# Kernel optimization log

Hardware: AMD Instinct MI355X
Metric: run time of the kernel (lower is better)

The kernel has to match this reference:

```python
import jax, jax.numpy as jnp
import numpy as np

D_MODEL = 1024
NUM_EXPERTS = 8
TOP_K = 2


def setup_inputs() -> dict:
    key = jax.random.key(0)
    k_x, k_g, k_w1, k_w2 = jax.random.split(key, 4)
    B, S, D, E = 4, 2048, D_MODEL, NUM_EXPERTS
    s_in = 1.0 / np.sqrt(D)
    s_hid = 1.0 / np.sqrt(4 * D)
    return {
        "x": jax.random.normal(k_x, (B, S, D), dtype=jnp.float32),
        "gate_w": jax.random.uniform(k_g, (E, D), jnp.float32, -s_in, s_in),
        "w1": jax.random.uniform(k_w1, (E, 4 * D, D), jnp.float32, -s_in, s_in),
        "w2": jax.random.uniform(k_w2, (E, D, 4 * D), jnp.float32, -s_hid, s_hid),
    }


def reference(x, gate_w, w1, w2):
    # x: [B,S,D]; gate_w: [E,D]; w1: [E,4D,D]; w2: [E,D,4D]
    gate_logits = jnp.einsum("bsd,ed->bse", x, gate_w)  # [B,S,E]
    top_v, top_i = jax.lax.top_k(gate_logits, TOP_K)     # [B,S,K]
    gates = jax.nn.softmax(top_v, axis=-1)               # [B,S,K]
    # combine weights per expert: [B,S,E]
    combine = jnp.sum(
        jax.nn.one_hot(top_i, NUM_EXPERTS, dtype=x.dtype) * gates[..., None],
        axis=-2,
    )
    out = jnp.zeros_like(x)
    for e in range(NUM_EXPERTS):
        h = jax.nn.relu(jnp.einsum("bsd,fd->bsf", x, w1[e]))   # [B,S,4D]
        y = jnp.einsum("bsf,df->bsd", h, w2[e])                # [B,S,D]
        out = out + combine[..., e, None] * y
    return out
```

## Files before the change

kernel.cpp:

```cpp
#include <hip/hip_runtime.h>
#include <hip/hip_bf16.h>
#include <stdint.h>

#define D_MODEL 1024
#define HDIM    4096
#define NE      8
#define MAXTILES 136

typedef __attribute__((ext_vector_type(8))) short short8;
typedef __attribute__((ext_vector_type(4))) float f32x4;
typedef __attribute__((ext_vector_type(2))) __bf16 bf16x2;
typedef __attribute__((ext_vector_type(4))) unsigned int uint4v;
typedef __attribute__((ext_vector_type(2))) unsigned int uint2v;

__device__ inline unsigned pk2(float a, float b) {
  bf16x2 v; v[0] = (__bf16)a; v[1] = (__bf16)b;
  return __builtin_bit_cast(unsigned, v);
}
__device__ inline unsigned short f2bf(float a) {
  __bf16 v = (__bf16)a;
  return __builtin_bit_cast(unsigned short, v);
}
__device__ inline void async16(const void* g, void* l) {
  __builtin_amdgcn_global_load_lds(
      (const __attribute__((address_space(1))) unsigned int*)g,
      (__attribute__((address_space(3))) unsigned int*)l, 16, 0, 0);
}

__global__ __launch_bounds__(256) void gate_kernel(
    const float* __restrict__ x, const float* __restrict__ gw,
    int* __restrict__ counts, int* __restrict__ tk_e, float* __restrict__ tk_g,
    unsigned short* __restrict__ xbf)
{
  const int t = blockIdx.x;
  const int tid = threadIdx.x;
  const float4 xv = ((const float4*)(x + (size_t)t * D_MODEL))[tid];
  if (xbf) {
    uint2v p; p[0] = pk2(xv.x, xv.y); p[1] = pk2(xv.z, xv.w);
    ((uint2v*)(xbf + (size_t)t * D_MODEL))[tid] = p;
  }
  float part[NE];
#pragma unroll
  for (int e = 0; e < NE; ++e) {
    const float4 gv = ((const float4*)(gw + e * D_MODEL))[tid];
    part[e] = xv.x * gv.x + xv.y * gv.y + xv.z * gv.z + xv.w * gv.w;
  }
#pragma unroll
  for (int off = 32; off > 0; off >>= 1)
#pragma unroll
    for (int e = 0; e < NE; ++e) part[e] += __shfl_down(part[e], off, 64);
  __shared__ float red[4][NE];
  const int wid = tid >> 6, lane = tid & 63;
  if (lane == 0)
    for (int e = 0; e < NE; ++e) red[wid][e] = part[e];
  __syncthreads();
  if (tid == 0) {
    float lg[NE];
    for (int e = 0; e < NE; ++e) lg[e] = red[0][e] + red[1][e] + red[2][e] + red[3][e];
    int e0 = 0;
    for (int e = 1; e < NE; ++e) if (lg[e] > lg[e0]) e0 = e;
    int e1 = (e0 == 0) ? 1 : 0;
    for (int e = 0; e < NE; ++e) { if (e == e0) continue; if (lg[e] > lg[e1]) e1 = e; }
    const float g0 = 1.0f / (1.0f + expf(lg[e1] - lg[e0]));
    tk_e[2*t] = e0; tk_e[2*t+1] = e1;
    tk_g[2*t] = g0; tk_g[2*t+1] = 1.0f - g0;
    atomicAdd(&counts[e0], 1);
    atomicAdd(&counts[e1], 1);
  }
}

__global__ void prefix_kernel(const int* __restrict__ counts,
                              int* __restrict__ cursor, int* __restrict__ offsets,
                              int* __restrict__ tiles, int* __restrict__ n_tiles) {
  if (threadIdx.x == 0) {
    int s = 0, n = 0;
    for (int e = 0; e < NE; ++e) {
      offsets[e] = s;
      const int nt = (counts[e] + 127) >> 7;
      for (int z = 0; z < nt; ++z) tiles[n++] = (e << 16) | z;
      s += counts[e];
      cursor[e] = 0;
    }
    *n_tiles = n;
  }
}

__global__ __launch_bounds__(256) void place_kernel(
    const int* __restrict__ tk_e, const float* __restrict__ tk_g,
    const int* __restrict__ offsets, int* __restrict__ cursor,
    int* __restrict__ token_of, float* __restrict__ gate_of, int T)
{
  const int t = blockIdx.x * 256 + threadIdx.x;
  if (t >= T) return;
  for (int k = 0; k < 2; ++k) {
    const int e = tk_e[2*t + k];
    const int pos = offsets[e] + atomicAdd(&cursor[e], 1);
    token_of[pos] = t;
    gate_of[pos] = tk_g[2*t + k];
  }
}

__global__ __launch_bounds__(256) void convert_kernel(
    const float* __restrict__ src, unsigned short* __restrict__ dst, long n4)
{
  long i = (long)blockIdx.x * 256 + threadIdx.x;
  const long stride = (long)gridDim.x * 256;
  for (; i < n4; i += stride) {
    const float4 v = ((const float4*)src)[i];
    uint2v p; p[0] = pk2(v.x, v.y); p[1] = pk2(v.z, v.w);
    ((uint2v*)dst)[i] = p;
  }
}

template<bool ABF, bool BBF>
__global__ __launch_bounds__(256) void gemm1_t(
    const float* __restrict__ xf, const unsigned short* __restrict__ xb,
    const float* __restrict__ w1f, const unsigned short* __restrict__ w1b,
    const int* __restrict__ counts, const int* __restrict__ offsets,
    const int* __restrict__ tiles, const int* __restrict__ n_tiles,
    const int* __restrict__ token_of, unsigned short* __restrict__ h)
{
  if ((int)blockIdx.x >= *n_tiles) return;
  const int desc = tiles[blockIdx.x];
  const int e = desc >> 16, zt = desc & 0xffff;
  const int ne = counts[e];
  const int off = offsets[e];
  const int p0 = off + zt * 128, pend = off + ne;
  const int f0 = blockIdx.y * 128;

  __shared__ __align__(16) short As[128 * 32];
  __shared__ __align__(16) short Bs[128 * 32];

  const int tid = threadIdx.x, lane = tid & 63, wid = tid >> 6;
  const int wm = (wid & 1) * 64, wn = (wid >> 1) * 64;
  const int lr = lane & 15, lq = lane >> 4;

  const unsigned short* aSrc0 = nullptr; const unsigned short* aSrc1 = nullptr;
  short* aDst0 = nullptr; short* aDst1 = nullptr;
  const float* aptrF = nullptr;
  if (ABF) {
    const int r0 = wid * 32 + (lane >> 2), r1 = r0 + 16;
    int i0 = p0 + r0; if (i0 >= pend) i0 = pend - 1;
    int i1 = p0 + r1; if (i1 >= pend) i1 = pend - 1;
    aSrc0 = xb + (size_t)token_of[i0] * D_MODEL + (lane & 3) * 8;
    aSrc1 = xb + (size_t)token_of[i1] * D_MODEL + (lane & 3) * 8;
    aDst0 = As + (wid * 2 + 0) * 512;
    aDst1 = As + (wid * 2 + 1) * 512;
  } else {
    const int r = tid >> 1, ch = tid & 1;
    int ip = p0 + r; if (ip >= pend) ip = pend - 1;
    aptrF = xf + (size_t)token_of[ip] * D_MODEL + ch * 16;
  }
  const unsigned short* bSrc0 = nullptr; const unsigned short* bSrc1 = nullptr;
  short* bDst0 = nullptr; short* bDst1 = nullptr;
  const float* bptrF = nullptr;
  if (BBF) {
    const unsigned short* w1be = w1b + (size_t)e * ((size_t)HDIM * D_MODEL);
    const int r0 = wid * 32 + (lane >> 2), r1 = r0 + 16;
    bSrc0 = w1be + (size_t)(f0 + r0) * D_MODEL + (lane & 3) * 8;
    bSrc1 = w1be + (size_t)(f0 + r1) * D_MODEL + (lane & 3) * 8;
    bDst0 = Bs + (wid * 2 + 0) * 512;
    bDst1 = Bs + (wid * 2 + 1) * 512;
  } else {
    const float* w1fe = w1f + (size_t)e * ((size_t)HDIM * D_MODEL);
    const int r = tid >> 1, ch = tid & 1;
    bptrF = w1fe + (size_t)(f0 + r) * D_MODEL + ch * 16;
  }
  const int rM = tid >> 1, chM = tid & 1;

  f32x4 acc[4][4];
#pragma unroll
  for (int i = 0; i < 4; ++i)
#pragma unroll
    for (int j = 0; j < 4; ++j) acc[i][j] = (f32x4){0.f, 0.f, 0.f, 0.f};

  for (int kk = 0; kk < D_MODEL; kk += 32) {
    float4 a0, a1, a2, a3, b0, b1, b2, b3;
    if (!ABF) {
      a0 = *(const float4*)(aptrF + kk);     a1 = *(const float4*)(aptrF + kk + 4);
      a2 = *(const float4*)(aptrF + kk + 8); a3 = *(const float4*)(aptrF + kk + 12);
    }
    if (!BBF) {
      b0 = *(const float4*)(bptrF + kk);     b1 = *(const float4*)(bptrF + kk + 4);
      b2 = *(const float4*)(bptrF + kk + 8); b3 = *(const float4*)(bptrF + kk + 12);
    }
    __syncthreads();
    if (ABF) {
      async16(aSrc0 + kk, aDst0);
      async16(aSrc1 + kk, aDst1);
    } else {
      uint4v wa0 = {pk2(a0.x,a0.y), pk2(a0.z,a0.w), pk2(a1.x,a1.y), pk2(a1.z,a1.w)};
      uint4v wa1 = {pk2(a2.x,a2.y), pk2(a2.z,a2.w), pk2(a3.x,a3.y), pk2(a3.z,a3.w)};
      *(uint4v*)&As[rM * 32 + chM * 16]     = wa0;
      *(uint4v*)&As[rM * 32 + chM * 16 + 8] = wa1;
    }
    if (BBF) {
      async16(bSrc0 + kk, bDst0);
      async16(bSrc1 + kk, bDst1);
    } else {
      uint4v wb0 = {pk2(b0.x,b0.y), pk2(b0.z,b0.w), pk2(b1.x,b1.y), pk2(b1.z,b1.w)};
      uint4v wb1 = {pk2(b2.x,b2.y), pk2(b2.z,b2.w), pk2(b3.x,b3.y), pk2(b3.z,b3.w)};
      *(uint4v*)&Bs[rM * 32 + chM * 16]     = wb0;
      *(uint4v*)&Bs[rM * 32 + chM * 16 + 8] = wb1;
    }
    __syncthreads();
    short8 af[4], bfr[4];
#pragma unroll
    for (int i = 0; i < 4; ++i) af[i]  = *(const short8*)&As[(wm + i*16 + lr) * 32 + lq * 8];
#pragma unroll
    for (int j = 0; j < 4; ++j) bfr[j] = *(const short8*)&Bs[(wn + j*16 + lr) * 32 + lq * 8];
#pragma unroll
    for (int i = 0; i < 4; ++i)
#pragma unroll
      for (int j = 0; j < 4; ++j)
        acc[i][j] = __builtin_amdgcn_mfma_f32_16x16x32_bf16(af[i], bfr[j], acc[i][j], 0, 0, 0);
  }

#pragma unroll
  for (int i = 0; i < 4; ++i) {
#pragma unroll
    for (int g = 0; g < 4; ++g) {
      const int m = wm + i*16 + lq*4 + g;
      const int pp = p0 + m;
      if (pp < pend) {
        unsigned short* hrow = h + (size_t)pp * HDIM + f0 + wn + lr;
#pragma unroll
        for (int j = 0; j < 4; ++j) {
          float v = acc[i][j][g];
          v = v > 0.f ? v : 0.f;
          hrow[j*16] = f2bf(v);
        }
      }
    }
  }
}

template<bool BBF>
__global__ __launch_bounds__(256) void gemm2_t(
    const unsigned short* __restrict__ h, const float* __restrict__ w2f,
    const unsigned short* __restrict__ w2b,
    const int* __restrict__ counts, const int* __restrict__ offsets,
    const int* __restrict__ tiles, const int* __restrict__ n_tiles,
    const int* __restrict__ token_of, const float* __restrict__ gate_of,
    float* __restrict__ out)
{
  if ((int)blockIdx.x >= *n_tiles) return;
  const int desc = tiles[blockIdx.x];
  const int e = desc >> 16, zt = desc & 0xffff;
  const int ne = counts[e];
  const int off = offsets[e];
  const int p0 = off + zt * 128, pend = off + ne;
  const int d0 = blockIdx.y * 128;

  __shared__ __align__(16) short As[128 * 32];
  __shared__ __align__(16) short Bs[128 * 32];

  const int tid = threadIdx.x, lane = tid & 63, wid = tid >> 6;
  const int wm = (wid & 1) * 64, wn = (wid >> 1) * 64;
  const int lr = lane & 15, lq = lane >> 4;

  const int rA0 = wid * 32 + (lane >> 2), rA1 = rA0 + 16;
  int iA0 = p0 + rA0; if (iA0 >= pend) iA0 = pend - 1;
  int iA1 = p0 + rA1; if (iA1 >= pend) iA1 = pend - 1;
  const unsigned short* aSrc0 = h + (size_t)iA0 * HDIM + (lane & 3) * 8;
  const unsigned short* aSrc1 = h + (size_t)iA1 * HDIM + (lane & 3) * 8;
  short* aDst0 = As + (wid * 2 + 0) * 512;
  short* aDst1 = As + (wid * 2 + 1) * 512;

  const unsigned short* bSrc0 = nullptr; const unsigned short* bSrc1 = nullptr;
  short* bDst0 = nullptr; short* bDst1 = nullptr;
  const float* bptrF = nullptr;
  if (BBF) {
    const unsigned short* w2be = w2b + (size_t)e * ((size_t)D_MODEL * HDIM);
    bSrc0 = w2be + (size_t)(d0 + rA0) * HDIM + (lane & 3) * 8;
    bSrc1 = w2be + (size_t)(d0 + rA1) * HDIM + (lane & 3) * 8;
    bDst0 = Bs + (wid * 2 + 0) * 512;
    bDst1 = Bs + (wid * 2 + 1) * 512;
  } else {
    const float* w2fe = w2f + (size_t)e * ((size_t)D_MODEL * HDIM);
    bptrF = w2fe + (size_t)(d0 + (tid >> 1)) * HDIM + (tid & 1) * 16;
  }
  const int rM = tid >> 1, chM = tid & 1;

  f32x4 acc[4][4];
#pragma unroll
  for (int i = 0; i < 4; ++i)
#pragma unroll
    for (int j = 0; j < 4; ++j) acc[i][j] = (f32x4){0.f, 0.f, 0.f, 0.f};

  for (int kk = 0; kk < HDIM; kk += 32) {
    float4 b0, b1, b2, b3;
    if (!BBF) {
      b0 = *(const float4*)(bptrF + kk);     b1 = *(const float4*)(bptrF + kk + 4);
      b2 = *(const float4*)(bptrF + kk + 8); b3 = *(const float4*)(bptrF + kk + 12);
    }
    __syncthreads();
    async16(aSrc0 + kk, aDst0);
    async16(aSrc1 + kk, aDst1);
    if (BBF) {
      async16(bSrc0 + kk, bDst0);
      async16(bSrc1 + kk, bDst1);
    } else {
      uint4v wb0 = {pk2(b0.x,b0.y), pk2(b0.z,b0.w), pk2(b1.x,b1.y), pk2(b1.z,b1.w)};
      uint4v wb1 = {pk2(b2.x,b2.y), pk2(b2.z,b2.w), pk2(b3.x,b3.y), pk2(b3.z,b3.w)};
      *(uint4v*)&Bs[rM * 32 + chM * 16]     = wb0;
      *(uint4v*)&Bs[rM * 32 + chM * 16 + 8] = wb1;
    }
    __syncthreads();
    short8 af[4], bfr[4];
#pragma unroll
    for (int i = 0; i < 4; ++i) af[i]  = *(const short8*)&As[(wm + i*16 + lr) * 32 + lq * 8];
#pragma unroll
    for (int j = 0; j < 4; ++j) bfr[j] = *(const short8*)&Bs[(wn + j*16 + lr) * 32 + lq * 8];
#pragma unroll
    for (int i = 0; i < 4; ++i)
#pragma unroll
      for (int j = 0; j < 4; ++j)
        acc[i][j] = __builtin_amdgcn_mfma_f32_16x16x32_bf16(af[i], bfr[j], acc[i][j], 0, 0, 0);
  }

#pragma unroll
  for (int i = 0; i < 4; ++i) {
#pragma unroll
    for (int g = 0; g < 4; ++g) {
      const int m = wm + i*16 + lq*4 + g;
      const int pp = p0 + m;
      if (pp < pend) {
        const int tok = token_of[pp];
        const float gv = gate_of[pp];
        float* orow = out + (size_t)tok * D_MODEL + d0 + wn + lr;
#pragma unroll
        for (int j = 0; j < 4; ++j)
          atomicAdd(&orow[j*16], gv * acc[i][j][g]);
      }
    }
  }
}

extern "C" void kernel_launch(void* const* d_in, const int* in_sizes, int n_in,
                              void* d_out, int out_size, void* d_ws, size_t ws_size,
                              hipStream_t stream)
{
  const float* x  = (const float*)d_in[0];
  const float* gw = (const float*)d_in[1];
  const float* w1 = (const float*)d_in[2];
  const float* w2 = (const float*)d_in[3];
  float* out = (float*)d_out;
  const int T = in_sizes[0] / D_MODEL;

  char* wsb = (char*)d_ws;
  int*   counts   = (int*)wsb;
  int*   cursor   = counts + 8;
  int*   offsets  = cursor + 8;
  int*   n_tiles  = offsets + 8;
  int*   tiles    = n_tiles + 1;
  int*   tk_e     = tiles + MAXTILES;
  float* tk_g     = (float*)(tk_e + 2*T);
  int*   token_of = (int*)(tk_g + 2*T);
  float* gate_of  = (float*)(token_of + 2*T);

  const size_t MB = 1u << 20;
  const size_t xbf_sz = (size_t)T * D_MODEL * 2;
  const size_t wbf_sz = (size_t)NE * HDIM * D_MODEL * 2;
  const size_t h_sz   = (size_t)(2*T) * HDIM * 2;

  const bool tierB = ws_size >= MB + xbf_sz + h_sz;
  const bool tierA = ws_size >= MB + xbf_sz + 2*wbf_sz + h_sz;

  unsigned short* xbf = tierB ? (unsigned short*)(wsb + MB) : nullptr;
  unsigned short* w1b = tierA ? (unsigned short*)(wsb + MB + xbf_sz) : nullptr;
  unsigned short* w2b = tierA ? (unsigned short*)(wsb + MB + xbf_sz + wbf_sz) : nullptr;
  unsigned short* h;
  if (tierA)      h = (unsigned short*)(wsb + MB + xbf_sz + 2*wbf_sz);
  else if (tierB) h = (unsigned short*)(wsb + MB + xbf_sz);
  else            h = (unsigned short*)(wsb + MB);

  hipMemsetAsync(d_ws, 0, 128, stream);
  hipMemsetAsync(d_out, 0, (size_t)out_size * sizeof(float), stream);

  gate_kernel<<<T, 256, 0, stream>>>(x, gw, counts, tk_e, tk_g, xbf);
  prefix_kernel<<<1, 64, 0, stream>>>(counts, cursor, offsets, tiles, n_tiles);
  place_kernel<<<(T + 255) / 256, 256, 0, stream>>>(tk_e, tk_g, offsets, cursor,
                                                    token_of, gate_of, T);
  if (tierA) {
    const long n4 = (long)NE * HDIM * D_MODEL / 4;
    convert_kernel<<<4096, 256, 0, stream>>>(w1, w1b, n4);
    convert_kernel<<<4096, 256, 0, stream>>>(w2, w2b, n4);
  }

  dim3 g1(MAXTILES, HDIM / 128, 1);
  dim3 g2(MAXTILES, D_MODEL / 128, 1);
  if (tierA) {
    gemm1_t<true, true><<<g1, 256, 0, stream>>>(x, xbf, w1, w1b, counts, offsets,
                                                tiles, n_tiles, token_of, h);
    gemm2_t<true><<<g2, 256, 0, stream>>>(h, w2, w2b, counts, offsets,
                                          tiles, n_tiles, token_of, gate_of, out);
  } else if (tierB) {
    gemm1_t<true, false><<<g1, 256, 0, stream>>>(x, xbf, w1, w1b, counts, offsets,
                                                 tiles, n_tiles, token_of, h);
    gemm2_t<false><<<g2, 256, 0, stream>>>(h, w2, w2b, counts, offsets,
                                           tiles, n_tiles, token_of, gate_of, out);
  } else {
    gemm1_t<false, false><<<g1, 256, 0, stream>>>(x, xbf, w1, w1b, counts, offsets,
                                                  tiles, n_tiles, token_of, h);
    gemm2_t<false><<<g2, 256, 0, stream>>>(h, w2, w2b, counts, offsets,
                                           tiles, n_tiles, token_of, gate_of, out);
  }
}
```

Baseline: 1.058 ms.

## Replace atomic scatter in expert GEMM2 with per-slot stores plus gather reduce

In the bf16-weights path, the second expert GEMM no longer atomically adds gated results into the output. It writes raw per-slot rows into a workspace buffer instead, and a new reduce kernel gathers each token's two slot rows through an inverse index and combines them with the gate weights. This removes the float atomics and the output memset, at the cost of writing and re-reading a large intermediate buffer. The buffer reuses workspace regions that are dead by then. The GEMM2 grid is also transposed so that blocks adjacent in launch order share the same token tile, which should improve L2 reuse of h.

```diff
diff --git a/kernel.cpp b/kernel.cpp
--- a/kernel.cpp
+++ b/kernel.cpp
@@ -88,7 +88,8 @@
 __global__ __launch_bounds__(256) void place_kernel(
     const int* __restrict__ tk_e, const float* __restrict__ tk_g,
     const int* __restrict__ offsets, int* __restrict__ cursor,
-    int* __restrict__ token_of, float* __restrict__ gate_of, int T)
+    int* __restrict__ token_of, float* __restrict__ gate_of,
+    int* __restrict__ inv, int T)
 {
   const int t = blockIdx.x * 256 + threadIdx.x;
   if (t >= T) return;
@@ -97,6 +98,7 @@
     const int pos = offsets[e] + atomicAdd(&cursor[e], 1);
     token_of[pos] = t;
     gate_of[pos] = tk_g[2*t + k];
+    inv[2*t + k] = pos;
   }
 }
 
@@ -110,6 +112,21 @@
     uint2v p; p[0] = pk2(v.x, v.y); p[1] = pk2(v.z, v.w);
     ((uint2v*)dst)[i] = p;
   }
+}
+
+__global__ __launch_bounds__(256) void reduce_kernel(
+    const float* __restrict__ y, const int* __restrict__ inv,
+    const float* __restrict__ tk_g, float* __restrict__ out)
+{
+  const int t = blockIdx.x;
+  const float g0 = tk_g[2*t], g1 = tk_g[2*t+1];
+  const float4* r0 = (const float4*)(y + (size_t)inv[2*t]     * D_MODEL);
+  const float4* r1 = (const float4*)(y + (size_t)inv[2*t + 1] * D_MODEL);
+  const float4 a = r0[threadIdx.x], b = r1[threadIdx.x];
+  float4 o;
+  o.x = g0*a.x + g1*b.x; o.y = g0*a.y + g1*b.y;
+  o.z = g0*a.z + g1*b.z; o.w = g0*a.w + g1*b.w;
+  ((float4*)(out + (size_t)t * D_MODEL))[threadIdx.x] = o;
 }
 
 template<bool ABF, bool BBF>
@@ -235,22 +252,22 @@
   }
 }
 
-template<bool BBF>
+template<bool BBF, bool USEY>
 __global__ __launch_bounds__(256) void gemm2_t(
     const unsigned short* __restrict__ h, const float* __restrict__ w2f,
     const unsigned short* __restrict__ w2b,
     const int* __restrict__ counts, const int* __restrict__ offsets,
     const int* __restrict__ tiles, const int* __restrict__ n_tiles,
     const int* __restrict__ token_of, const float* __restrict__ gate_of,
-    float* __restrict__ out)
-{
-  if ((int)blockIdx.x >= *n_tiles) return;
-  const int desc = tiles[blockIdx.x];
+    float* __restrict__ outy)
+{
+  if ((int)blockIdx.y >= *n_tiles) return;
+  const int desc = tiles[blockIdx.y];
   const int e = desc >> 16, zt = desc & 0xffff;
   const int ne = counts[e];
   const int off = offsets[e];
   const int p0 = off + zt * 128, pend = off + ne;
-  const int d0 = blockIdx.y * 128;
+  const int d0 = blockIdx.x * 128;
 
   __shared__ __align__(16) short As[128 * 32];
   __shared__ __align__(16) short Bs[128 * 32];
@@ -326,12 +343,19 @@
       const int m = wm + i*16 + lq*4 + g;
       const int pp = p0 + m;
       if (pp < pend) {
-        const int tok = token_of[pp];
-        const float gv = gate_of[pp];
-        float* orow = out + (size_t)tok * D_MODEL + d0 + wn + lr;
-#pragma unroll
-        for (int j = 0; j < 4; ++j)
-          atomicAdd(&orow[j*16], gv * acc[i][j][g]);
+        if (USEY) {
+          float* yrow = outy + (size_t)pp * D_MODEL + d0 + wn + lr;
+#pragma unroll
+          for (int j = 0; j < 4; ++j)
+            yrow[j*16] = acc[i][j][g];
+        } else {
+          const int tok = token_of[pp];
+          const float gv = gate_of[pp];
+          float* orow = outy + (size_t)tok * D_MODEL + d0 + wn + lr;
+#pragma unroll
+          for (int j = 0; j < 4; ++j)
+            atomicAdd(&orow[j*16], gv * acc[i][j][g]);
+        }
       }
     }
   }
@@ -358,6 +382,7 @@
   float* tk_g     = (float*)(tk_e + 2*T);
   int*   token_of = (int*)(tk_g + 2*T);
   float* gate_of  = (float*)(token_of + 2*T);
+  int*   inv      = (int*)(gate_of + 2*T);
 
   const size_t MB = 1u << 20;
   const size_t xbf_sz = (size_t)T * D_MODEL * 2;
@@ -374,14 +399,16 @@
   if (tierA)      h = (unsigned short*)(wsb + MB + xbf_sz + 2*wbf_sz);
   else if (tierB) h = (unsigned short*)(wsb + MB + xbf_sz);
   else            h = (unsigned short*)(wsb + MB);
+  float* y = (float*)(wsb + MB);
 
   hipMemsetAsync(d_ws, 0, 128, stream);
-  hipMemsetAsync(d_out, 0, (size_t)out_size * sizeof(float), stream);
+  if (!tierA)
+    hipMemsetAsync(d_out, 0, (size_t)out_size * sizeof(float), stream);
 
   gate_kernel<<<T, 256, 0, stream>>>(x, gw, counts, tk_e, tk_g, xbf);
   prefix_kernel<<<1, 64, 0, stream>>>(counts, cursor, offsets, tiles, n_tiles);
   place_kernel<<<(T + 255) / 256, 256, 0, stream>>>(tk_e, tk_g, offsets, cursor,
-                                                    token_of, gate_of, T);
+                                                    token_of, gate_of, inv, T);
   if (tierA) {
     const long n4 = (long)NE * HDIM * D_MODEL / 4;
     convert_kernel<<<4096, 256, 0, stream>>>(w1, w1b, n4);
@@ -389,21 +416,22 @@
   }
 
   dim3 g1(MAXTILES, HDIM / 128, 1);
-  dim3 g2(MAXTILES, D_MODEL / 128, 1);
+  dim3 g2(D_MODEL / 128, MAXTILES, 1);
   if (tierA) {
     gemm1_t<true, true><<<g1, 256, 0, stream>>>(x, xbf, w1, w1b, counts, offsets,
                                                 tiles, n_tiles, token_of, h);
-    gemm2_t<true><<<g2, 256, 0, stream>>>(h, w2, w2b, counts, offsets,
-                                          tiles, n_tiles, token_of, gate_of, out);
+    gemm2_t<true, true><<<g2, 256, 0, stream>>>(h, w2, w2b, counts, offsets,
+                                                tiles, n_tiles, token_of, gate_of, y);
+    reduce_kernel<<<T, 256, 0, stream>>>(y, inv, tk_g, out);
   } else if (tierB) {
     gemm1_t<true, false><<<g1, 256, 0, stream>>>(x, xbf, w1, w1b, counts, offsets,
                                                  tiles, n_tiles, token_of, h);
-    gemm2_t<false><<<g2, 256, 0, stream>>>(h, w2, w2b, counts, offsets,
-                                           tiles, n_tiles, token_of, gate_of, out);
+    gemm2_t<false, false><<<g2, 256, 0, stream>>>(h, w2, w2b, counts, offsets,
+                                                  tiles, n_tiles, token_of, gate_of, out);
   } else {
     gemm1_t<false, false><<<g1, 256, 0, stream>>>(x, xbf, w1, w1b, counts, offsets,
                                                   tiles, n_tiles, token_of, h);
-    gemm2_t<false><<<g2, 256, 0, stream>>>(h, w2, w2b, counts, offsets,
-                                           tiles, n_tiles, token_of, gate_of, out);
-  }
-}
+    gemm2_t<false, false><<<g2, 256, 0, stream>>>(h, w2, w2b, counts, offsets,
+                                                  tiles, n_tiles, token_of, gate_of, out);
+  }
+}
```

Measured after the change: 1.123 ms. 1.06x slower.
